# Optimization experiments

Measured on AMD Instinct MI355X. Metric: run time of the kernel, lower is better.

The kernel has to match this reference:

```python
import jax, jax.numpy as jnp
import numpy as np
from jax import lax

NMS_THRESHOLD = 0.7
POST_NMS_TOP_N = 1000
N_BOXES = 2048
CAP = 8  # max vertices of intersection of two convex quads
EPS = 1e-8


def _cross(a, b):
    return a[..., 0] * b[..., 1] - a[..., 1] * b[..., 0]


def _corners(b):
    # b: (5,) [xc, yc, w, h, theta] -> (4,2) CCW corners
    xc, yc, w, h, t = b[0], b[1], b[2], b[3], b[4]
    c, s = jnp.cos(t), jnp.sin(t)
    lx = jnp.array([-0.5, 0.5, 0.5, -0.5], dtype=b.dtype) * w
    ly = jnp.array([-0.5, -0.5, 0.5, 0.5], dtype=b.dtype) * h
    x = xc + lx * c - ly * s
    y = yc + lx * s + ly * c
    return jnp.stack([x, y], axis=-1)


def _clip(poly, n, p0, p1):
    # Sutherland-Hodgman clip of poly (CAP,2) with n valid verts against
    # half-plane to the left of edge p0->p1 (CCW interior).
    idx = jnp.arange(CAP)
    valid = idx < n
    nsafe = jnp.maximum(n, 1)
    prev = poly[(idx + nsafe - 1) % nsafe]
    e = p1 - p0
    d_cur = _cross(e, poly - p0)
    d_prev = _cross(e, prev - p0)
    cur_in = d_cur >= 0.0
    prev_in = d_prev >= 0.0
    denom = d_prev - d_cur
    denom = jnp.where(jnp.abs(denom) < EPS, EPS, denom)
    t = d_prev / denom
    ipt = prev + t[:, None] * (poly - prev)  # edge/half-plane intersection
    # per input vertex emit: [crossing point, current vertex]
    pts = jnp.stack([ipt, poly], axis=1).reshape(2 * CAP, 2)
    vmask = jnp.stack([valid & (cur_in != prev_in), valid & cur_in], axis=1).reshape(2 * CAP)
    order = jnp.argsort(~vmask, stable=True)  # compact valid points to front
    new_n = jnp.minimum(jnp.sum(vmask).astype(jnp.int32), CAP)
    return pts[order][:CAP], new_n


def _inter_area(b1, b2):
    poly = jnp.zeros((CAP, 2), dtype=b1.dtype).at[:4].set(_corners(b1))
    n = jnp.int32(4)
    r2 = _corners(b2)
    for k in range(4):
        poly, n = _clip(poly, n, r2[k], r2[(k + 1) % 4])
    idx = jnp.arange(CAP)
    valid = idx < n
    nxt = (idx + 1) % jnp.maximum(n, 1)
    area = 0.5 * jnp.abs(jnp.sum(jnp.where(valid, _cross(poly, poly[nxt]), 0.0)))
    return jnp.where(n >= 3, area, 0.0)


def _pairwise_iou(boxes):
    inter = jax.vmap(lambda b1: jax.vmap(lambda b2: _inter_area(b1, b2))(boxes))(boxes)
    area = boxes[:, 2] * boxes[:, 3]
    return inter / (area[:, None] + area[None, :] - inter + EPS)


def _greedy(iou, thresh, topn):
    n = iou.shape[0]
    js = jnp.arange(n, dtype=jnp.int32)

    def body(i, st):
        keep, cnt, sup = st
        take = jnp.logical_and(jnp.logical_not(sup[i]), cnt < topn)
        keep = jnp.where(take, keep.at[cnt].set(i), keep)
        sup = sup | (take & (iou[i] >= thresh) & (js > i))
        return keep, cnt + take.astype(jnp.int32), sup

    keep0 = jnp.full((topn,), -1, dtype=jnp.int32)
    keep, _, _ = lax.fori_loop(0, n, body, (keep0, jnp.int32(0), jnp.zeros((n,), dtype=bool)))
    return keep


def setup_inputs() -> dict:
    key = jax.random.key(0)
    k1, k2, k3 = jax.random.split(key, 3)
    xy = jax.random.uniform(k1, (N_BOXES, 2), minval=0.0, maxval=1024.0)
    wh = jax.random.uniform(k2, (N_BOXES, 2), minval=8.0, maxval=128.0)
    th = jax.random.uniform(k3, (N_BOXES, 1), minval=-np.pi / 2, maxval=np.pi / 2)
    r_boxes = jnp.concatenate([xy, wh, th], axis=1).astype(jnp.float32)
    return {"r_boxes": r_boxes}


def reference(r_boxes):
    # boxes assumed pre-sorted by score (as in the original module)
    iou = _pairwise_iou(r_boxes)
    keep = _greedy(iou, NMS_THRESHOLD, POST_NMS_TOP_N)  # (post_nms_top_n,), -1 padded
    return keep
```

## Files before the change

kernel.cpp:

```cpp
#include <hip/hip_runtime.h>
#include <hip/hip_bf16.h>

#define CAP 8
#define EPSF 1e-8f
#define NMS_THR 0.7f
#define TOPN 1000
#define ITILE 16
#define QCAP (256 * ITILE)
#define CAPR 480

#define GLOBAL_AS __attribute__((address_space(1)))
#define LDS_AS    __attribute__((address_space(3)))

__device__ __forceinline__ float rect_inter_area_cs(
    float xc1, float yc1, float w1, float h1, float c1, float s1,
    float xc2, float yc2, float w2, float h2, float c2, float s2)
{
    float px[CAP], py[CAP];
    {
        float lx0 = -0.5f * w1, lx1 = 0.5f * w1;
        float ly0 = -0.5f * h1, ly1 = 0.5f * h1;
        px[0] = xc1 + lx0 * c1 - ly0 * s1;  py[0] = yc1 + lx0 * s1 + ly0 * c1;
        px[1] = xc1 + lx1 * c1 - ly0 * s1;  py[1] = yc1 + lx1 * s1 + ly0 * c1;
        px[2] = xc1 + lx1 * c1 - ly1 * s1;  py[2] = yc1 + lx1 * s1 + ly1 * c1;
        px[3] = xc1 + lx0 * c1 - ly1 * s1;  py[3] = yc1 + lx0 * s1 + ly1 * c1;
#pragma unroll
        for (int s2i = 4; s2i < CAP; ++s2i) { px[s2i] = 0.f; py[s2i] = 0.f; }
    }
    float qx[4], qy[4];
    {
        float lx0 = -0.5f * w2, lx1 = 0.5f * w2;
        float ly0 = -0.5f * h2, ly1 = 0.5f * h2;
        qx[0] = xc2 + lx0 * c2 - ly0 * s2;  qy[0] = yc2 + lx0 * s2 + ly0 * c2;
        qx[1] = xc2 + lx1 * c2 - ly0 * s2;  qy[1] = yc2 + lx1 * s2 + ly0 * c2;
        qx[2] = xc2 + lx1 * c2 - ly1 * s2;  qy[2] = yc2 + lx1 * s2 + ly1 * c2;
        qx[3] = xc2 + lx0 * c2 - ly1 * s2;  qy[3] = yc2 + lx0 * s2 + ly1 * c2;
    }

    int n = 4;
#pragma unroll
    for (int e = 0; e < 4; ++e) {
        float p0x = qx[e], p0y = qy[e];
        float ex = qx[(e + 1) & 3] - p0x, ey = qy[(e + 1) & 3] - p0y;

        float pxp = px[0], pyp = py[0];
#pragma unroll
        for (int s = 1; s < CAP; ++s)
            if (s == n - 1) { pxp = px[s]; pyp = py[s]; }
        float dp = ex * (pyp - p0y) - ey * (pxp - p0x);

        float nx_[CAP], ny_[CAP];
#pragma unroll
        for (int s = 0; s < CAP; ++s) { nx_[s] = 0.f; ny_[s] = 0.f; }
        int m = 0;

#pragma unroll
        for (int k = 0; k < CAP; ++k) {
            bool act = (k < n);
            float pxc = px[k], pyc = py[k];
            float dc = ex * (pyc - p0y) - ey * (pxc - p0x);
            bool cin = (dc >= 0.0f), pin = (dp >= 0.0f);

            float den = dp - dc;
            den = (fabsf(den) < EPSF) ? EPSF : den;
            float t = dp / den;
            float ix = pxp + t * (pxc - pxp);
            float iy = pyp + t * (pyc - pyp);

            bool emit_cross = act && (cin != pin);
            if (emit_cross) {
#pragma unroll
                for (int s = 0; s < CAP; ++s)
                    if (s == m) { nx_[s] = ix; ny_[s] = iy; }
                ++m;
            }
            bool emit_cur = act && cin;
            if (emit_cur) {
#pragma unroll
                for (int s = 0; s < CAP; ++s)
                    if (s == m) { nx_[s] = pxc; ny_[s] = pyc; }
                ++m;
            }
            if (act) { pxp = pxc; pyp = pyc; dp = dc; }
        }
        n = (m < CAP) ? m : CAP;
#pragma unroll
        for (int s = 0; s < CAP; ++s) { px[s] = nx_[s]; py[s] = ny_[s]; }
    }

    if (n < 3) return 0.0f;
    float s = 0.0f;
#pragma unroll
    for (int k = 0; k < CAP; ++k) {
        if (k < n) {
            float nxk = px[(k + 1) & (CAP - 1)];
            float nyk = py[(k + 1) & (CAP - 1)];
            if (k == n - 1) { nxk = px[0]; nyk = py[0]; }
            s += px[k] * nyk - py[k] * nxk;
        }
    }
    return 0.5f * fabsf(s);
}

__global__ __launch_bounds__(256)
void init_kernel(const float* __restrict__ boxes, float4* __restrict__ box8,
                 ulonglong2* __restrict__ maskv,
                 unsigned long long* __restrict__ summary,
                 int n, int rows_total, int words)
{
    int t = blockIdx.x * 256 + threadIdx.x;
    if (t < rows_total) {
        ulonglong2 z; z.x = 0ULL; z.y = 0ULL;
        ulonglong2* p = maskv + (size_t)t * (words >> 1);
        for (int k = 0; k < (words >> 1); ++k) p[k] = z;
    }
    if (t < 64) summary[t] = 0ULL;
    if (t < n) {
        const float* b = boxes + (size_t)t * 5;
        float x = b[0], y = b[1], w = b[2], h = b[3], th = b[4];
        box8[2 * t]     = make_float4(x, y, w, h);
        box8[2 * t + 1] = make_float4(cosf(th), sinf(th),
                                      0.5f * sqrtf(w * w + h * h), w * h);
    }
}

__global__ __launch_bounds__(256)
void filter_kernel(const float4* __restrict__ box8,
                   unsigned long long* __restrict__ mask,
                   unsigned long long* __restrict__ summary,
                   int n, int words)
{
    const int jt = blockIdx.x, it = blockIdx.y;
    const int i0 = it * ITILE;
    if (i0 >= jt * 256 + 255) return;
    const int j = jt * 256 + threadIdx.x;

    __shared__ float4 atile[2 * ITILE];
    __shared__ unsigned int q[QCAP];
    __shared__ int qcnt;

    if (threadIdx.x == 0) qcnt = 0;
    if (threadIdx.x < 2 * ITILE) {
        int src = 2 * i0 + threadIdx.x;
        atile[threadIdx.x] = (src < 2 * n) ? box8[src]
                                           : make_float4(0.f, 0.f, 0.f, 0.f);
    }
    __syncthreads();

    float4 B0, B1;
    bool jok = (j < n);
    if (jok) { B0 = box8[2 * j]; B1 = box8[2 * j + 1]; }
    else     { B0 = make_float4(0,0,0,0); B1 = make_float4(0,0,0,0); }

#pragma unroll
    for (int ii = 0; ii < ITILE; ++ii) {
        int i = i0 + ii;
        float4 A0 = atile[2 * ii], A1 = atile[2 * ii + 1];
        bool pass = jok && (j > i) && (i < n);
        float dx = A0.x - B0.x, dy = A0.y - B0.y;
        float rr = A1.z + B1.z + 1e-2f;
        pass = pass && (dx * dx + dy * dy <= rr * rr);
        float amin = fminf(A1.w, B1.w), amax = fmaxf(A1.w, B1.w);
        pass = pass && (amin >= 0.699f * amax);
        if (pass) {
            int idx = atomicAdd(&qcnt, 1);
            q[idx] = ((unsigned int)i << 16) | (unsigned int)j;
        }
    }
    __syncthreads();

    int qn = qcnt;
    for (int t = threadIdx.x; t < qn; t += 256) {
        unsigned int pk = q[t];
        int i2 = (int)(pk >> 16), j2 = (int)(pk & 0xffffu);
        float4 A0 = box8[2 * i2], A1 = box8[2 * i2 + 1];
        float4 C0 = box8[2 * j2], C1 = box8[2 * j2 + 1];
        float a1 = A1.w, a2 = C1.w;
        float inter = rect_inter_area_cs(A0.x, A0.y, A0.z, A0.w, A1.x, A1.y,
                                         C0.x, C0.y, C0.z, C0.w, C1.x, C1.y);
        float iou = inter / (a1 + a2 - inter + EPSF);
        if (iou >= NMS_THR) {
            atomicOr(&mask[(size_t)i2 * words + (j2 >> 6)], 1ULL << (j2 & 63));
            atomicOr(&summary[i2 >> 6], 1ULL << (i2 & 63));
        }
    }
}

__device__ __forceinline__ unsigned long long rl64(unsigned long long v, int l) {
    unsigned int lo = (unsigned int)__builtin_amdgcn_readlane((int)(unsigned int)v, l);
    unsigned int hi = (unsigned int)__builtin_amdgcn_readlane((int)(v >> 32), l);
    return ((unsigned long long)hi << 32) | lo;
}

__global__ __launch_bounds__(64, 1)
void greedy_kernel(const unsigned long long* __restrict__ mask,
                   const unsigned long long* __restrict__ summary,
                   int* __restrict__ keep, int n, int words)
{
    __shared__ __align__(16) unsigned long long rowdat[CAPR * 32];
    __shared__ unsigned int rowlist[CAPR];
    const int lane = threadIdx.x;
    const int chunks = (n + 63) >> 6;

    unsigned long long szv = (lane < chunks) ? summary[lane] : 0ULL;

    int pc = __popcll(szv);
    int pref = pc;
#pragma unroll
    for (int d = 1; d < 64; d <<= 1) {
        int t = __shfl_up(pref, d);
        if (lane >= d) pref += t;
    }
    int base_excl = pref - pc;
    int R = __shfl(pref, chunks - 1);

    {
        unsigned long long m = szv;
        int s = base_excl;
        while (m && s < CAPR) {
            int k = (int)__builtin_ctzll(m);
            m &= m - 1;
            rowlist[s] = (unsigned int)((lane << 6) + k);
            ++s;
        }
    }
    __syncthreads();

    int Rc = (R < CAPR) ? R : CAPR;
    if (Rc > 0) {
        int nins = (Rc + 3) >> 2;
        for (int t = 0; t < nins; ++t) {
            int slot = (t << 2) + (lane >> 4);
            int cs = (slot < Rc) ? slot : (Rc - 1);
            unsigned int row = rowlist[cs];
            const char* src = (const char*)(mask + (size_t)row * words)
                            + (size_t)(lane & 15) * 16;
            char* dst = (char*)rowdat + (size_t)t * 1024;
            __builtin_amdgcn_global_load_lds(
                (const GLOBAL_AS unsigned int*)src,
                (LDS_AS unsigned int*)dst, 16, 0, 0);
        }
    }
    asm volatile("s_waitcnt vmcnt(0)" ::: "memory");
    __builtin_amdgcn_sched_barrier(0);

    unsigned long long acc = 0ULL;
    int cnt = 0;

    for (int c = 0; c < chunks; ++c) {
        if (cnt >= TOPN) break;
        const int base = c << 6;
        unsigned long long cw = rl64(acc, c);
        unsigned long long nzc = rl64(szv, c);
        unsigned long long valid =
            (n - base >= 64) ? ~0ULL : ((1ULL << (n - base)) - 1ULL);
        unsigned long long cand = ~cw & valid;
        int rem = TOPN - cnt;

        unsigned long long kmask;
        if ((nzc & cand) == 0ULL && __popcll(cand) <= rem) {
            kmask = cand;
        } else {
            int bexc = __builtin_amdgcn_readlane(base_excl, c);
            unsigned long long D = 0ULL;
            if ((nzc >> lane) & 1ULL) {
                int slot = bexc +
                    (int)__popcll(nzc & ((lane == 0) ? 0ULL
                                         : ((~0ULL) >> (64 - lane))));
                D = (slot < CAPR)
                    ? rowdat[(size_t)slot * 32 + c]
                    : mask[(size_t)(base + lane) * words + c];
            }
            unsigned long long intra = __ballot((D & cand) != 0ULL);
            if ((intra & cand) == 0ULL && __popcll(cand) <= rem) {
                kmask = cand;
            } else {
                kmask = 0ULL;
                int cl = cnt;
#pragma unroll
                for (int k = 0; k < 64; ++k) {
                    if (!((cw >> k) & 1ULL) && cl < TOPN && (base + k) < n) {
                        cw |= rl64(D, k);
                        kmask |= (1ULL << k);
                        ++cl;
                    }
                }
            }
        }

        if ((kmask >> lane) & 1ULL)
            keep[cnt + __popcll(kmask & ((1ULL << lane) - 1ULL))] = base + lane;
        cnt += __popcll(kmask);

        unsigned long long orrows = kmask & nzc;
        if (orrows) {
            int bexc = __builtin_amdgcn_readlane(base_excl, c);
            while (orrows) {
                int r = (int)__builtin_ctzll(orrows);
                orrows &= orrows - 1ULL;
                int slot = bexc +
                    (int)__popcll(nzc & ((r == 0) ? 0ULL
                                         : ((~0ULL) >> (64 - r))));
                unsigned long long v = (slot < CAPR)
                    ? rowdat[(size_t)slot * 32 + (lane & 31)]
                    : mask[(size_t)(base + r) * words + (lane & 31)];
                acc |= v;
            }
        }
    }

    for (int t = cnt + lane; t < TOPN; t += 64) keep[t] = -1;
}

extern "C" void kernel_launch(void* const* d_in, const int* in_sizes, int n_in,
                              void* d_out, int out_size, void* d_ws, size_t ws_size,
                              hipStream_t stream) {
    const float* boxes = (const float*)d_in[0];
    int n = in_sizes[0] / 5;
    int words = (n + 63) / 64;
    int chunks = (n + 63) / 64;
    int rows_total = chunks * 64;
    int* keep = (int*)d_out;

    unsigned long long* mask = (unsigned long long*)d_ws;
    size_t mask_alloc = (size_t)rows_total * words * 8;
    unsigned long long* summary =
        (unsigned long long*)((char*)d_ws + mask_alloc);
    float4* box8 = (float4*)((char*)d_ws + mask_alloc + 512);

    init_kernel<<<(rows_total + 255) / 256, 256, 0, stream>>>(
        boxes, box8, (ulonglong2*)mask, summary, n, rows_total, words);

    dim3 grid((n + 255) / 256, (n + ITILE - 1) / ITILE);
    filter_kernel<<<grid, 256, 0, stream>>>(box8, mask, summary, n, words);
    greedy_kernel<<<1, 64, 0, stream>>>(mask, summary, keep, n, words);
}
```

Baseline: 28.96 us.

## Fuse init, filter and greedy NMS into one cooperative persistent kernel

Replaces the three launches (init, pairwise filter, greedy scan) with one cooperative kernel of 256 persistent blocks. Grid-wide syncs separate the phases, and the blocks walk a linearised list of non-empty (j-tile, i-tile) pairs. Only block 0 runs the greedy scan afterwards. CAPR is halved so the shared buffer fits alongside the filter queue, which means more suppression rows fall back to global memory. The aim is to remove launch gaps between kernels, at the cost of grid-sync overhead, per-tile index decoding, and dropping the LDS staging of the i-tile.

```diff
diff --git a/kernel.cpp b/kernel.cpp
--- a/kernel.cpp
+++ b/kernel.cpp
@@ -1,5 +1,8 @@
 #include <hip/hip_runtime.h>
+#include <hip/hip_cooperative_groups.h>
 #include <hip/hip_bf16.h>
+
+namespace cg = cooperative_groups;
 
 #define CAP 8
 #define EPSF 1e-8f
@@ -7,7 +10,8 @@
 #define TOPN 1000
 #define ITILE 16
 #define QCAP (256 * ITILE)
-#define CAPR 480
+#define CAPR 240
+#define NBLOCKS 256
 
 #define GLOBAL_AS __attribute__((address_space(1)))
 #define LDS_AS    __attribute__((address_space(3)))
@@ -102,214 +106,230 @@
     return 0.5f * fabsf(s);
 }
 
-__global__ __launch_bounds__(256)
-void init_kernel(const float* __restrict__ boxes, float4* __restrict__ box8,
-                 ulonglong2* __restrict__ maskv,
-                 unsigned long long* __restrict__ summary,
-                 int n, int rows_total, int words)
-{
-    int t = blockIdx.x * 256 + threadIdx.x;
-    if (t < rows_total) {
-        ulonglong2 z; z.x = 0ULL; z.y = 0ULL;
-        ulonglong2* p = maskv + (size_t)t * (words >> 1);
-        for (int k = 0; k < (words >> 1); ++k) p[k] = z;
-    }
-    if (t < 64) summary[t] = 0ULL;
-    if (t < n) {
-        const float* b = boxes + (size_t)t * 5;
-        float x = b[0], y = b[1], w = b[2], h = b[3], th = b[4];
-        box8[2 * t]     = make_float4(x, y, w, h);
-        box8[2 * t + 1] = make_float4(cosf(th), sinf(th),
-                                      0.5f * sqrtf(w * w + h * h), w * h);
-    }
-}
-
-__global__ __launch_bounds__(256)
-void filter_kernel(const float4* __restrict__ box8,
-                   unsigned long long* __restrict__ mask,
-                   unsigned long long* __restrict__ summary,
-                   int n, int words)
-{
-    const int jt = blockIdx.x, it = blockIdx.y;
-    const int i0 = it * ITILE;
-    if (i0 >= jt * 256 + 255) return;
-    const int j = jt * 256 + threadIdx.x;
-
-    __shared__ float4 atile[2 * ITILE];
-    __shared__ unsigned int q[QCAP];
-    __shared__ int qcnt;
-
-    if (threadIdx.x == 0) qcnt = 0;
-    if (threadIdx.x < 2 * ITILE) {
-        int src = 2 * i0 + threadIdx.x;
-        atile[threadIdx.x] = (src < 2 * n) ? box8[src]
-                                           : make_float4(0.f, 0.f, 0.f, 0.f);
-    }
-    __syncthreads();
-
-    float4 B0, B1;
-    bool jok = (j < n);
-    if (jok) { B0 = box8[2 * j]; B1 = box8[2 * j + 1]; }
-    else     { B0 = make_float4(0,0,0,0); B1 = make_float4(0,0,0,0); }
-
-#pragma unroll
-    for (int ii = 0; ii < ITILE; ++ii) {
-        int i = i0 + ii;
-        float4 A0 = atile[2 * ii], A1 = atile[2 * ii + 1];
-        bool pass = jok && (j > i) && (i < n);
-        float dx = A0.x - B0.x, dy = A0.y - B0.y;
-        float rr = A1.z + B1.z + 1e-2f;
-        pass = pass && (dx * dx + dy * dy <= rr * rr);
-        float amin = fminf(A1.w, B1.w), amax = fmaxf(A1.w, B1.w);
-        pass = pass && (amin >= 0.699f * amax);
-        if (pass) {
-            int idx = atomicAdd(&qcnt, 1);
-            q[idx] = ((unsigned int)i << 16) | (unsigned int)j;
-        }
-    }
-    __syncthreads();
-
-    int qn = qcnt;
-    for (int t = threadIdx.x; t < qn; t += 256) {
-        unsigned int pk = q[t];
-        int i2 = (int)(pk >> 16), j2 = (int)(pk & 0xffffu);
-        float4 A0 = box8[2 * i2], A1 = box8[2 * i2 + 1];
-        float4 C0 = box8[2 * j2], C1 = box8[2 * j2 + 1];
-        float a1 = A1.w, a2 = C1.w;
-        float inter = rect_inter_area_cs(A0.x, A0.y, A0.z, A0.w, A1.x, A1.y,
-                                         C0.x, C0.y, C0.z, C0.w, C1.x, C1.y);
-        float iou = inter / (a1 + a2 - inter + EPSF);
-        if (iou >= NMS_THR) {
-            atomicOr(&mask[(size_t)i2 * words + (j2 >> 6)], 1ULL << (j2 & 63));
-            atomicOr(&summary[i2 >> 6], 1ULL << (i2 & 63));
-        }
-    }
-}
-
 __device__ __forceinline__ unsigned long long rl64(unsigned long long v, int l) {
     unsigned int lo = (unsigned int)__builtin_amdgcn_readlane((int)(unsigned int)v, l);
     unsigned int hi = (unsigned int)__builtin_amdgcn_readlane((int)(v >> 32), l);
     return ((unsigned long long)hi << 32) | lo;
 }
 
-__global__ __launch_bounds__(64, 1)
-void greedy_kernel(const unsigned long long* __restrict__ mask,
-                   const unsigned long long* __restrict__ summary,
-                   int* __restrict__ keep, int n, int words)
+__global__ __launch_bounds__(256, 1)
+void fused_kernel(const float* __restrict__ boxes, float4* __restrict__ box8,
+                  unsigned long long* __restrict__ mask,
+                  unsigned long long* __restrict__ summary,
+                  int* __restrict__ keep, int n, int words)
 {
-    __shared__ __align__(16) unsigned long long rowdat[CAPR * 32];
-    __shared__ unsigned int rowlist[CAPR];
-    const int lane = threadIdx.x;
-    const int chunks = (n + 63) >> 6;
-
-    unsigned long long szv = (lane < chunks) ? summary[lane] : 0ULL;
-
-    int pc = __popcll(szv);
-    int pref = pc;
-#pragma unroll
-    for (int d = 1; d < 64; d <<= 1) {
-        int t = __shfl_up(pref, d);
-        if (lane >= d) pref += t;
-    }
-    int base_excl = pref - pc;
-    int R = __shfl(pref, chunks - 1);
+    __shared__ __align__(16) unsigned char smem[CAPR * 256 + CAPR * 4];
+    __shared__ int qcnt;
+
+    const int tid = threadIdx.x;
+    const int gid = blockIdx.x * 256 + tid;
+    cg::grid_group grid = cg::this_grid();
+
+    const int rows_total = ((n + 63) >> 6) << 6;
+    for (int t = gid; t < rows_total * words; t += NBLOCKS * 256)
+        mask[t] = 0ULL;
+    if (gid < 64) summary[gid] = 0ULL;
+    if (gid < n) {
+        const float* b = boxes + (size_t)gid * 5;
+        float x = b[0], y = b[1], w = b[2], h = b[3], th = b[4];
+        box8[2 * gid]     = make_float4(x, y, w, h);
+        box8[2 * gid + 1] = make_float4(cosf(th), sinf(th),
+                                        0.5f * sqrtf(w * w + h * h), w * h);
+    }
+    grid.sync();
 
     {
-        unsigned long long m = szv;
-        int s = base_excl;
-        while (m && s < CAPR) {
-            int k = (int)__builtin_ctzll(m);
-            m &= m - 1;
-            rowlist[s] = (unsigned int)((lane << 6) + k);
-            ++s;
-        }
-    }
-    __syncthreads();
-
-    int Rc = (R < CAPR) ? R : CAPR;
-    if (Rc > 0) {
-        int nins = (Rc + 3) >> 2;
-        for (int t = 0; t < nins; ++t) {
-            int slot = (t << 2) + (lane >> 4);
-            int cs = (slot < Rc) ? slot : (Rc - 1);
-            unsigned int row = rowlist[cs];
-            const char* src = (const char*)(mask + (size_t)row * words)
-                            + (size_t)(lane & 15) * 16;
-            char* dst = (char*)rowdat + (size_t)t * 1024;
-            __builtin_amdgcn_global_load_lds(
-                (const GLOBAL_AS unsigned int*)src,
-                (LDS_AS unsigned int*)dst, 16, 0, 0);
-        }
-    }
-    asm volatile("s_waitcnt vmcnt(0)" ::: "memory");
-    __builtin_amdgcn_sched_barrier(0);
-
-    unsigned long long acc = 0ULL;
-    int cnt = 0;
-
-    for (int c = 0; c < chunks; ++c) {
-        if (cnt >= TOPN) break;
-        const int base = c << 6;
-        unsigned long long cw = rl64(acc, c);
-        unsigned long long nzc = rl64(szv, c);
-        unsigned long long valid =
-            (n - base >= 64) ? ~0ULL : ((1ULL << (n - base)) - 1ULL);
-        unsigned long long cand = ~cw & valid;
-        int rem = TOPN - cnt;
-
-        unsigned long long kmask;
-        if ((nzc & cand) == 0ULL && __popcll(cand) <= rem) {
-            kmask = cand;
-        } else {
-            int bexc = __builtin_amdgcn_readlane(base_excl, c);
-            unsigned long long D = 0ULL;
-            if ((nzc >> lane) & 1ULL) {
-                int slot = bexc +
-                    (int)__popcll(nzc & ((lane == 0) ? 0ULL
-                                         : ((~0ULL) >> (64 - lane))));
-                D = (slot < CAPR)
-                    ? rowdat[(size_t)slot * 32 + c]
-                    : mask[(size_t)(base + lane) * words + c];
-            }
-            unsigned long long intra = __ballot((D & cand) != 0ULL);
-            if ((intra & cand) == 0ULL && __popcll(cand) <= rem) {
+        unsigned int* q = (unsigned int*)smem;
+
+        const int itiles = (n + ITILE - 1) / ITILE;
+        const int jtiles = (n + 255) / 256;
+        int T = 0;
+        for (int q2 = 0; q2 < jtiles; ++q2) {
+            int c2 = (q2 * 256 + 254) / ITILE + 1;
+            T += (c2 < itiles) ? c2 : itiles;
+        }
+
+        for (int L = blockIdx.x; L < T; L += NBLOCKS) {
+            int L2 = L, jt = -1, it = 0;
+            for (int q2 = 0; q2 < jtiles; ++q2) {
+                int c2 = (q2 * 256 + 254) / ITILE + 1;
+                c2 = (c2 < itiles) ? c2 : itiles;
+                if (jt < 0) {
+                    if (L2 < c2) { jt = q2; it = L2; }
+                    else L2 -= c2;
+                }
+            }
+            const int i0 = it * ITILE;
+            const int j = jt * 256 + tid;
+
+            if (tid == 0) qcnt = 0;
+            __syncthreads();
+
+            float4 B0, B1;
+            bool jok = (j < n);
+            if (jok) { B0 = box8[2 * j]; B1 = box8[2 * j + 1]; }
+            else     { B0 = make_float4(0,0,0,0); B1 = make_float4(0,0,0,0); }
+
+#pragma unroll
+            for (int ii = 0; ii < ITILE; ++ii) {
+                int i = i0 + ii;
+                if (i < n) {
+                    float4 A0 = box8[2 * i];
+                    float4 A1 = box8[2 * i + 1];
+                    bool pass = jok && (j > i);
+                    float dx = A0.x - B0.x, dy = A0.y - B0.y;
+                    float rr = A1.z + B1.z + 1e-2f;
+                    pass = pass && (dx * dx + dy * dy <= rr * rr);
+                    float amin = fminf(A1.w, B1.w), amax = fmaxf(A1.w, B1.w);
+                    pass = pass && (amin >= 0.699f * amax);
+                    if (pass) {
+                        int idx = atomicAdd(&qcnt, 1);
+                        q[idx] = ((unsigned int)i << 16) | (unsigned int)j;
+                    }
+                }
+            }
+            __syncthreads();
+
+            int qn = qcnt;
+            for (int t = tid; t < qn; t += 256) {
+                unsigned int pk = q[t];
+                int i2 = (int)(pk >> 16), j2 = (int)(pk & 0xffffu);
+                float4 A0 = box8[2 * i2], A1 = box8[2 * i2 + 1];
+                float4 C0 = box8[2 * j2], C1 = box8[2 * j2 + 1];
+                float a1 = A1.w, a2 = C1.w;
+                float inter = rect_inter_area_cs(
+                    A0.x, A0.y, A0.z, A0.w, A1.x, A1.y,
+                    C0.x, C0.y, C0.z, C0.w, C1.x, C1.y);
+                float iou = inter / (a1 + a2 - inter + EPSF);
+                if (iou >= NMS_THR) {
+                    atomicOr(&mask[(size_t)i2 * words + (j2 >> 6)],
+                             1ULL << (j2 & 63));
+                    atomicOr(&summary[i2 >> 6], 1ULL << (i2 & 63));
+                }
+            }
+            __syncthreads();
+        }
+    }
+    grid.sync();
+
+    if (blockIdx.x != 0) return;
+    {
+        unsigned long long* rowdat = (unsigned long long*)smem;
+        unsigned int* rowlist = (unsigned int*)(smem + CAPR * 256);
+        const int lane = tid & 63;
+        if (tid >= 64) return;
+        const int chunks = (n + 63) >> 6;
+
+        unsigned long long szv = (lane < chunks) ? summary[lane] : 0ULL;
+
+        int pc = __popcll(szv);
+        int pref = pc;
+#pragma unroll
+        for (int d = 1; d < 64; d <<= 1) {
+            int t = __shfl_up(pref, d);
+            if (lane >= d) pref += t;
+        }
+        int base_excl = pref - pc;
+        int R = __shfl(pref, chunks - 1);
+
+        {
+            unsigned long long m = szv;
+            int s = base_excl;
+            while (m && s < CAPR) {
+                int k = (int)__builtin_ctzll(m);
+                m &= m - 1;
+                rowlist[s] = (unsigned int)((lane << 6) + k);
+                ++s;
+            }
+        }
+        __builtin_amdgcn_s_barrier();
+
+        int Rc = (R < CAPR) ? R : CAPR;
+        if (Rc > 0) {
+            int nins = (Rc + 3) >> 2;
+            for (int t = 0; t < nins; ++t) {
+                int slot = (t << 2) + (lane >> 4);
+                int cs = (slot < Rc) ? slot : (Rc - 1);
+                unsigned int row = rowlist[cs];
+                const char* src = (const char*)(mask + (size_t)row * words)
+                                + (size_t)(lane & 15) * 16;
+                char* dst = (char*)rowdat + (size_t)t * 1024;
+                __builtin_amdgcn_global_load_lds(
+                    (const GLOBAL_AS unsigned int*)src,
+                    (LDS_AS unsigned int*)dst, 16, 0, 0);
+            }
+        }
+        asm volatile("s_waitcnt vmcnt(0)" ::: "memory");
+        __builtin_amdgcn_sched_barrier(0);
+
+        unsigned long long acc = 0ULL;
+        int cnt = 0;
+
+        for (int c = 0; c < chunks; ++c) {
+            if (cnt >= TOPN) break;
+            const int base = c << 6;
+            unsigned long long cw = rl64(acc, c);
+            unsigned long long nzc = rl64(szv, c);
+            unsigned long long valid =
+                (n - base >= 64) ? ~0ULL : ((1ULL << (n - base)) - 1ULL);
+            unsigned long long cand = ~cw & valid;
+            int rem = TOPN - cnt;
+
+            unsigned long long kmask;
+            if ((nzc & cand) == 0ULL && __popcll(cand) <= rem) {
                 kmask = cand;
             } else {
-                kmask = 0ULL;
-                int cl = cnt;
-#pragma unroll
-                for (int k = 0; k < 64; ++k) {
-                    if (!((cw >> k) & 1ULL) && cl < TOPN && (base + k) < n) {
-                        cw |= rl64(D, k);
-                        kmask |= (1ULL << k);
-                        ++cl;
+                int bexc = __builtin_amdgcn_readlane(base_excl, c);
+                unsigned long long D = 0ULL;
+                if ((nzc >> lane) & 1ULL) {
+                    int slot = bexc +
+                        (int)__popcll(nzc & ((lane == 0) ? 0ULL
+                                             : ((~0ULL) >> (64 - lane))));
+                    D = (slot < CAPR)
+                        ? rowdat[(size_t)slot * 32 + c]
+                        : mask[(size_t)(base + lane) * words + c];
+                }
+                unsigned long long intra = __ballot((D & cand) != 0ULL);
+                if ((intra & cand) == 0ULL && __popcll(cand) <= rem) {
+                    kmask = cand;
+                } else {
+                    kmask = 0ULL;
+                    int cl = cnt;
+#pragma unroll
+                    for (int k = 0; k < 64; ++k) {
+                        if (!((cw >> k) & 1ULL) && cl < TOPN && (base + k) < n) {
+                            cw |= rl64(D, k);
+                            kmask |= (1ULL << k);
+                            ++cl;
+                        }
                     }
                 }
             }
-        }
-
-        if ((kmask >> lane) & 1ULL)
-            keep[cnt + __popcll(kmask & ((1ULL << lane) - 1ULL))] = base + lane;
-        cnt += __popcll(kmask);
-
-        unsigned long long orrows = kmask & nzc;
-        if (orrows) {
-            int bexc = __builtin_amdgcn_readlane(base_excl, c);
-            while (orrows) {
-                int r = (int)__builtin_ctzll(orrows);
-                orrows &= orrows - 1ULL;
-                int slot = bexc +
-                    (int)__popcll(nzc & ((r == 0) ? 0ULL
-                                         : ((~0ULL) >> (64 - r))));
-                unsigned long long v = (slot < CAPR)
-                    ? rowdat[(size_t)slot * 32 + (lane & 31)]
-                    : mask[(size_t)(base + r) * words + (lane & 31)];
-                acc |= v;
-            }
-        }
-    }
-
-    for (int t = cnt + lane; t < TOPN; t += 64) keep[t] = -1;
+
+            if ((kmask >> lane) & 1ULL)
+                keep[cnt + __popcll(kmask & ((1ULL << lane) - 1ULL))] =
+                    base + lane;
+            cnt += __popcll(kmask);
+
+            unsigned long long orrows = kmask & nzc;
+            if (orrows) {
+                int bexc = __builtin_amdgcn_readlane(base_excl, c);
+                while (orrows) {
+                    int r = (int)__builtin_ctzll(orrows);
+                    orrows &= orrows - 1ULL;
+                    int slot = bexc +
+                        (int)__popcll(nzc & ((r == 0) ? 0ULL
+                                             : ((~0ULL) >> (64 - r))));
+                    unsigned long long v = (slot < CAPR)
+                        ? rowdat[(size_t)slot * 32 + (lane & 31)]
+                        : mask[(size_t)(base + r) * words + (lane & 31)];
+                    acc |= v;
+                }
+            }
+        }
+
+        for (int t = cnt + lane; t < TOPN; t += 64) keep[t] = -1;
+    }
 }
 
 extern "C" void kernel_launch(void* const* d_in, const int* in_sizes, int n_in,
@@ -318,8 +338,7 @@
     const float* boxes = (const float*)d_in[0];
     int n = in_sizes[0] / 5;
     int words = (n + 63) / 64;
-    int chunks = (n + 63) / 64;
-    int rows_total = chunks * 64;
+    int rows_total = ((n + 63) / 64) * 64;
     int* keep = (int*)d_out;
 
     unsigned long long* mask = (unsigned long long*)d_ws;
@@ -328,10 +347,8 @@
         (unsigned long long*)((char*)d_ws + mask_alloc);
     float4* box8 = (float4*)((char*)d_ws + mask_alloc + 512);
 
-    init_kernel<<<(rows_total + 255) / 256, 256, 0, stream>>>(
-        boxes, box8, (ulonglong2*)mask, summary, n, rows_total, words);
-
-    dim3 grid((n + 255) / 256, (n + ITILE - 1) / ITILE);
-    filter_kernel<<<grid, 256, 0, stream>>>(box8, mask, summary, n, words);
-    greedy_kernel<<<1, 64, 0, stream>>>(mask, summary, keep, n, words);
+    void* args[] = {(void*)&boxes, (void*)&box8, (void*)&mask,
+                    (void*)&summary, (void*)&keep, (void*)&n, (void*)&words};
+    hipLaunchCooperativeKernel((const void*)fused_kernel, dim3(NBLOCKS),
+                               dim3(256), args, 0, stream);
 }
```

After: 90.67 us. 3.13x slower.
